# Kernel tuning notes

Measured on AMD Instinct MI355X. Metric: run time of the kernel, lower is better.

The kernel has to match this reference:

```python
import jax, jax.numpy as jnp
import numpy as np


def setup_inputs() -> dict:
    key = jax.random.key(0)
    B, T, D, H = 32, 1600, 512, 512
    # variable lengths, nonincreasing (PackedSequence convention)
    lengths = np.array([T - 25 * i for i in range(B)])            # 1600 .. 825
    bs = (lengths[None, :] > np.arange(T)[:, None]).sum(1)        # batch_sizes[t], nonincreasing
    t_idx = np.repeat(np.arange(T), bs)                           # packed element -> timestep
    b_idx = np.concatenate([np.arange(b) for b in bs])            # packed element -> batch row
    mask = np.arange(B)[None, :] < bs[:, None]                    # [T,B] active mask
    total = int(bs.sum())                                         # 38800
    ks = jax.random.split(key, 7)
    s = 1.0 / np.sqrt(H)
    return {
        "packed_data": jax.random.normal(ks[0], (total, D), jnp.float32),
        "h0": jax.random.normal(ks[1], (B, H), jnp.float32),
        "c0": jax.random.normal(ks[2], (B, H), jnp.float32),
        "w_ih": jax.random.uniform(ks[3], (4 * H, D), jnp.float32, -s, s),
        "w_hh": jax.random.uniform(ks[4], (4 * H, H), jnp.float32, -s, s),
        "b_ih": jax.random.uniform(ks[5], (4 * H,), jnp.float32, -s, s),
        "b_hh": jax.random.uniform(ks[6], (4 * H,), jnp.float32, -s, s),
        "t_idx": jnp.asarray(t_idx, jnp.int32),
        "b_idx": jnp.asarray(b_idx, jnp.int32),
        "mask": jnp.asarray(mask),
    }


def reference(packed_data, h0, c0, w_ih, w_hh, b_ih, b_hh, t_idx, b_idx, mask):
    # Reverse LSTM over a packed variable-length batch.
    # Equivalent math to the torch loop: process timesteps T-1 .. 0; a row's
    # hidden stays at its initial value until the row becomes active.
    T, B = mask.shape
    D = packed_data.shape[1]
    # unpack to padded [T,B,D] (zeros at inactive slots; never read for output)
    padded = jnp.zeros((T, B, D), packed_data.dtype).at[t_idx, b_idx].set(packed_data)

    def step(carry, xm):
        h, c = carry
        x, m = xm                                   # x:[B,D], m:[B]
        gates = x @ w_ih.T + b_ih + h @ w_hh.T + b_hh   # [B,4H]
        i, f, g, o = jnp.split(gates, 4, axis=-1)
        c_new = jax.nn.sigmoid(f) * c + jax.nn.sigmoid(i) * jnp.tanh(g)
        h_new = jax.nn.sigmoid(o) * jnp.tanh(c_new)
        m2 = m[:, None]
        # inactive rows keep their initial hidden until they enter the batch
        return (jnp.where(m2, h_new, h0), jnp.where(m2, c_new, c0)), h_new

    (hT, cT), outs = jax.lax.scan(step, (h0, c0), (padded[::-1], mask[::-1]))
    outs = outs[::-1]                               # [T,B,H], time-forward order
    packed_out = outs[t_idx, b_idx]                 # repack [total,H]
    return packed_out, hT, cT
```

## Files before the change

kernel.cpp:

```cpp
#include <hip/hip_runtime.h>
#include <hip/hip_bf16.h>
#include <stdint.h>

typedef __attribute__((ext_vector_type(8))) short bf16x8;
typedef __attribute__((ext_vector_type(4))) float f32x4;
typedef __attribute__((ext_vector_type(4))) int int4v;
typedef unsigned long long u64;

#define DD 512
#define HH 512
#define BB 32

__device__ __forceinline__ unsigned short f2bf(float f) {
  unsigned u = __float_as_uint(f);
  u += 0x7fffu + ((u >> 16) & 1u);
  return (unsigned short)(u >> 16);
}
__device__ __forceinline__ int pk2(float a, float b) {
  return (int)((unsigned)f2bf(a) | ((unsigned)f2bf(b) << 16));
}
__device__ __forceinline__ float bf2f(unsigned short v) {
  return __uint_as_float((unsigned)v << 16);
}
__device__ __forceinline__ float sigf(float x) { return 1.f / (1.f + __expf(-x)); }
__device__ __forceinline__ float tanhfast(float x) {
  float e = __expf(fminf(fmaxf(2.f * x, -60.f), 60.f));
  return (e - 1.f) / (e + 1.f);
}

__global__ void init_state(u64* hbuf, const float* __restrict__ h0, int* L) {
  int i = blockIdx.x * blockDim.x + threadIdx.x;
  if (i < 32) L[i] = 0;
  if (i < 16384) {
    int g = i >> 13, p = (i >> 12) & 1, m = (i >> 8) & 15, q = i & 255;
    u64 v;
    if (p == 0) {
      int b = g * 16 + m;
      unsigned lo = f2bf(h0[(size_t)b * HH + 2 * q]);
      unsigned hi = f2bf(h0[(size_t)b * HH + 2 * q + 1]);
      v = (u64)(lo | (hi << 16));
    } else {
      v = 0xFFFFFFFF00000000ull;
    }
    hbuf[i] = v;
  }
}

__global__ void init_idx(const int* __restrict__ t_idx, const int* __restrict__ b_idx,
                         int* rowstart, int* L, int total) {
  int r = blockIdx.x * blockDim.x + threadIdx.x;
  if (r >= total) return;
  int t = t_idx[r];
  if (r == 0 || t_idx[r - 1] != t) rowstart[t] = r;
  atomicMax(&L[b_idx[r]], t + 1);
}

__global__ __launch_bounds__(256, 2)
void gx_gemm(const float* __restrict__ X, const float* __restrict__ w_ih,
             const float* __restrict__ b_ih, const float* __restrict__ b_hh,
             unsigned short* __restrict__ GX, int total)
{
  const int ct = blockIdx.x & 7;
  const int rt = blockIdx.x >> 3;
  const int r0 = rt * 64;
  const int j0 = ct * 256;
  const int tid = threadIdx.x;
  const int lane = tid & 63, wv = tid >> 6;
  const int ul = lane & 15, kc = lane >> 4;

  __shared__ unsigned short As[64 * 64];
  __shared__ unsigned short Bs[256 * 64];
  char* As_c = (char*)As;
  char* Bs_c = (char*)Bs;

  f32x4 acc[4][4];
#pragma unroll
  for (int mf = 0; mf < 4; mf++)
#pragma unroll
    for (int nf = 0; nf < 4; nf++) acc[mf][nf] = (f32x4){0.f, 0.f, 0.f, 0.f};

  const int arow_s = tid >> 2;
  const int akq = (tid & 3) * 16;
  const size_t arow_g = (size_t)min(r0 + arow_s, total - 1);
  const int ab = arow_s * 128 + akq * 2, asw = (arow_s & 7) << 4;
  const int bcol = tid;
  const int bb = bcol * 128, bsw = (bcol & 7) << 4;

  for (int ch = 0; ch < 8; ch++) {
    const int k0 = ch * 64;
    {
      const f32x4* ap = (const f32x4*)(X + arow_g * DD + k0 + akq);
      f32x4 a0 = ap[0], a1 = ap[1], a2 = ap[2], a3 = ap[3];
      int4v p0 = {pk2(a0[0], a0[1]), pk2(a0[2], a0[3]), pk2(a1[0], a1[1]), pk2(a1[2], a1[3])};
      int4v p1 = {pk2(a2[0], a2[1]), pk2(a2[2], a2[3]), pk2(a3[0], a3[1]), pk2(a3[2], a3[3])};
      *(int4v*)(As_c + (ab ^ asw)) = p0;
      *(int4v*)(As_c + ((ab + 16) ^ asw)) = p1;
    }
    {
      const f32x4* bp = (const f32x4*)(w_ih + (size_t)(j0 + bcol) * DD + k0);
#pragma unroll
      for (int q = 0; q < 4; q++) {
        f32x4 b0 = bp[4 * q], b1 = bp[4 * q + 1], b2 = bp[4 * q + 2], b3 = bp[4 * q + 3];
        int4v p0 = {pk2(b0[0], b0[1]), pk2(b0[2], b0[3]), pk2(b1[0], b1[1]), pk2(b1[2], b1[3])};
        int4v p1 = {pk2(b2[0], b2[1]), pk2(b2[2], b2[3]), pk2(b3[0], b3[1]), pk2(b3[2], b3[3])};
        *(int4v*)(Bs_c + ((bb + q * 32) ^ bsw)) = p0;
        *(int4v*)(Bs_c + ((bb + q * 32 + 16) ^ bsw)) = p1;
      }
    }
    __syncthreads();
#pragma unroll
    for (int ks = 0; ks < 2; ks++) {
      bf16x8 bfr[4], afr[4];
#pragma unroll
      for (int nf = 0; nf < 4; nf++) {
        int col = wv * 64 + nf * 16 + ul;
        bfr[nf] = *(const bf16x8*)(Bs_c + ((col * 128 + ks * 64 + kc * 16) ^ ((col & 7) << 4)));
      }
#pragma unroll
      for (int mf = 0; mf < 4; mf++) {
        int row = mf * 16 + ul;
        afr[mf] = *(const bf16x8*)(As_c + ((row * 128 + ks * 64 + kc * 16) ^ ((row & 7) << 4)));
      }
#pragma unroll
      for (int mf = 0; mf < 4; mf++)
#pragma unroll
        for (int nf = 0; nf < 4; nf++)
          acc[mf][nf] = __builtin_amdgcn_mfma_f32_16x16x32_bf16(afr[mf], bfr[nf], acc[mf][nf], 0, 0, 0);
    }
    __syncthreads();
  }
#pragma unroll
  for (int nf = 0; nf < 4; nf++) {
    int c = j0 + wv * 64 + nf * 16 + ul;
    float bias = b_ih[c] + b_hh[c];
#pragma unroll
    for (int mf = 0; mf < 4; mf++)
#pragma unroll
      for (int r = 0; r < 4; r++) {
        int row = r0 + mf * 16 + kc * 4 + r;
        if (row < total) GX[(size_t)row * 2048 + c] = f2bf(acc[mf][nf][r] + bias);
      }
  }
}

__global__ __launch_bounds__(512, 2)
void lstm_gx(const float* __restrict__ h0, const float* __restrict__ c0,
             const float* __restrict__ w_hh,
             const int* __restrict__ rowstart, const int* __restrict__ L,
             u64* hbuf, const unsigned short* __restrict__ GX,
             float* out, int total)
{
  const int tid = threadIdx.x;
  const int bid = blockIdx.x;
  const int g = bid & 1;
  const int k = bid >> 1;
  const int lane = tid & 63;
  const int wave = tid >> 6;
  const int gate = wave & 3;
  const int cs = wave >> 2;
  const int ul = lane & 15;
  const int kc = lane >> 4;
  const int u0 = k * 32;
  const int j = gate * 512 + u0 + cs * 16 + ul;

  __shared__ unsigned short h_st[16 * HH];
  __shared__ float gl[4][16][33];

  bf16x8 wfb[16];
#pragma unroll
  for (int kk = 0; kk < 16; kk++) {
    const float* pb = w_hh + (size_t)j * HH + kk * 32 + kc * 8;
    bf16x8 vb;
#pragma unroll
    for (int e = 0; e < 8; e++) vb[e] = (short)f2bf(pb[e]);
    wfb[kk] = vb;
  }

  const int mC = tid >> 5;
  const int uC = tid & 31;
  const int bcell = g * 16 + mC;
  const int uu = u0 + uC;
  const int Lc = L[bcell];
  float c_reg = c0[(size_t)bcell * HH + uu];
  const float c0c = c_reg;
  const float h0c = h0[(size_t)bcell * HH + uu];

  int t0 = 0;
#pragma unroll
  for (int m = 0; m < 16; m++) t0 = max(t0, L[g * 16 + m]);
  t0 -= 1;
  const int S = t0 + 1;

  u64* hb_g = hbuf + g * 8192;
  const size_t hT_off = (size_t)total * HH;
  const size_t cT_off = hT_off + (size_t)BB * HH;

  char* hst_c = (char*)h_st;
  const int gr = (mC + k) & 15;
  const int gc = (uC + 2 * k) & 31;
  const int hbyte = gr * 1024 + gc * 32, hsw = (gr & 7) << 4;
  const int arow = ul * 1024, aswz = (ul & 7) << 4;

  unsigned short gx0 = 0, gx1 = 0, gx2 = 0, gx3 = 0;
  if (t0 < Lc) {
    const unsigned short* gp = GX + (size_t)(rowstart[t0] + bcell) * 2048 + uu;
    gx0 = gp[0]; gx1 = gp[512]; gx2 = gp[1024]; gx3 = gp[1536];
  }

  for (int s = 0, t = t0; s < S; s++, t--) {
    const bool act = (t < Lc);
    const u64* src = hb_g + (size_t)((s & 1) * 4096) + gr * 256 + gc * 8;
    int4v c0v, c1v, c2v, c3v;
    asm volatile(
      "global_load_dwordx4 %0, %4, off sc0 sc1\n\t"
      "global_load_dwordx4 %1, %5, off sc0 sc1\n\t"
      "global_load_dwordx4 %2, %6, off sc0 sc1\n\t"
      "global_load_dwordx4 %3, %7, off sc0 sc1"
      : "=&v"(c0v), "=&v"(c1v), "=&v"(c2v), "=&v"(c3v)
      : "v"(src), "v"(src + 2), "v"(src + 4), "v"(src + 6)
      : "memory");
    asm volatile("s_waitcnt vmcnt(0)" ::: "memory");
    __builtin_amdgcn_sched_barrier(0);
    const unsigned want = (unsigned)s;
    int spins = 0;
    while (!(((unsigned)c0v[1] == want) & ((unsigned)c0v[3] == want) &
             ((unsigned)c1v[1] == want) & ((unsigned)c1v[3] == want) &
             ((unsigned)c2v[1] == want) & ((unsigned)c2v[3] == want) &
             ((unsigned)c3v[1] == want) & ((unsigned)c3v[3] == want))) {
      if (++spins < 4096) {
        asm volatile(
          "global_load_dwordx4 %0, %4, off sc0 sc1\n\t"
          "global_load_dwordx4 %1, %5, off sc0 sc1\n\t"
          "global_load_dwordx4 %2, %6, off sc0 sc1\n\t"
          "global_load_dwordx4 %3, %7, off sc0 sc1\n\t"
          "s_waitcnt vmcnt(0)"
          : "=&v"(c0v), "=&v"(c1v), "=&v"(c2v), "=&v"(c3v)
          : "v"(src), "v"(src + 2), "v"(src + 4), "v"(src + 6)
          : "memory");
        __builtin_amdgcn_sched_barrier(0);
      } else {
        u64 a0 = __hip_atomic_load(src + 0, __ATOMIC_RELAXED, __HIP_MEMORY_SCOPE_AGENT);
        u64 a1 = __hip_atomic_load(src + 1, __ATOMIC_RELAXED, __HIP_MEMORY_SCOPE_AGENT);
        u64 a2 = __hip_atomic_load(src + 2, __ATOMIC_RELAXED, __HIP_MEMORY_SCOPE_AGENT);
        u64 a3 = __hip_atomic_load(src + 3, __ATOMIC_RELAXED, __HIP_MEMORY_SCOPE_AGENT);
        u64 a4 = __hip_atomic_load(src + 4, __ATOMIC_RELAXED, __HIP_MEMORY_SCOPE_AGENT);
        u64 a5 = __hip_atomic_load(src + 5, __ATOMIC_RELAXED, __HIP_MEMORY_SCOPE_AGENT);
        u64 a6 = __hip_atomic_load(src + 6, __ATOMIC_RELAXED, __HIP_MEMORY_SCOPE_AGENT);
        u64 a7 = __hip_atomic_load(src + 7, __ATOMIC_RELAXED, __HIP_MEMORY_SCOPE_AGENT);
        c0v = (int4v){(int)a0, (int)(a0 >> 32), (int)a1, (int)(a1 >> 32)};
        c1v = (int4v){(int)a2, (int)(a2 >> 32), (int)a3, (int)(a3 >> 32)};
        c2v = (int4v){(int)a4, (int)(a4 >> 32), (int)a5, (int)(a5 >> 32)};
        c3v = (int4v){(int)a6, (int)(a6 >> 32), (int)a7, (int)(a7 >> 32)};
      }
    }

    {
      int4v d0 = {c0v[0], c0v[2], c1v[0], c1v[2]};
      int4v d1 = {c2v[0], c2v[2], c3v[0], c3v[2]};
      *(int4v*)(hst_c + (hbyte ^ hsw)) = d0;
      *(int4v*)(hst_c + ((hbyte + 16) ^ hsw)) = d1;
    }
    unsigned short ngx0 = 0, ngx1 = 0, ngx2 = 0, ngx3 = 0;
    if (t > 0 && (t - 1) < Lc) {
      const unsigned short* gp = GX + (size_t)(rowstart[t - 1] + bcell) * 2048 + uu;
      ngx0 = gp[0]; ngx1 = gp[512]; ngx2 = gp[1024]; ngx3 = gp[1536];
    }
    __syncthreads();

    f32x4 C = {0.f, 0.f, 0.f, 0.f};
    f32x4 C2 = {0.f, 0.f, 0.f, 0.f};
#pragma unroll
    for (int kk = 0; kk < 8; kk++) {
      bf16x8 A0 = *(const bf16x8*)(hst_c + ((arow + (2 * kk) * 64 + kc * 16) ^ aswz));
      bf16x8 A1 = *(const bf16x8*)(hst_c + ((arow + (2 * kk + 1) * 64 + kc * 16) ^ aswz));
      C  = __builtin_amdgcn_mfma_f32_16x16x32_bf16(A0, wfb[2 * kk], C, 0, 0, 0);
      C2 = __builtin_amdgcn_mfma_f32_16x16x32_bf16(A1, wfb[2 * kk + 1], C2, 0, 0, 0);
    }
#pragma unroll
    for (int r = 0; r < 4; r++) gl[gate][kc * 4 + r][cs * 16 + ul] = C[r] + C2[r];
    __syncthreads();

    float gi = gl[0][mC][uC] + bf2f(gx0);
    float gf = gl[1][mC][uC] + bf2f(gx1);
    float gg = gl[2][mC][uC] + bf2f(gx2);
    float go = gl[3][mC][uC] + bf2f(gx3);
    float iv = sigf(gi), fv = sigf(gf), gv = tanhfast(gg), ov = sigf(go);
    float cn = fv * c_reg + iv * gv;
    float hn = ov * tanhfast(cn);
    float hp = act ? hn : h0c;
    c_reg = act ? cn : c0c;

    {
      unsigned hbf = (unsigned)f2bf(hp);
      unsigned v1 = __shfl_down(hbf, 1);
      if ((uC & 1) == 0) {
        u64 val = ((u64)(unsigned)(s + 1) << 32) | (hbf & 0xffffu) | ((v1 & 0xffffu) << 16);
        u64* dst = hb_g + (size_t)(((s + 1) & 1) * 4096) + mC * 256 + k * 16 + (uC >> 1);
        __hip_atomic_store(dst, val, __ATOMIC_RELAXED, __HIP_MEMORY_SCOPE_AGENT);
      }
    }
    if (act) {
      const int rst = rowstart[t];
      out[(size_t)(rst + bcell) * HH + uu] = hn;
      if (t == 0) {
        out[hT_off + (size_t)bcell * HH + uu] = hn;
        out[cT_off + (size_t)bcell * HH + uu] = cn;
      }
    }
    gx0 = ngx0; gx1 = ngx1; gx2 = ngx2; gx3 = ngx3;
  }
}

__global__ __launch_bounds__(512, 2)
void lstm_fused(const float* __restrict__ X, const float* __restrict__ h0,
                const float* __restrict__ c0, const float* __restrict__ w_ih,
                const float* __restrict__ w_hh, const float* __restrict__ b_ih,
                const float* __restrict__ b_hh, const int* __restrict__ rowstart,
                const int* __restrict__ L, u64* hbuf,
                float* out, int total)
{
  const int tid = threadIdx.x;
  const int bid = blockIdx.x;
  const int g = bid & 1;
  const int k = bid >> 1;
  const int lane = tid & 63;
  const int wave = tid >> 6;
  const int gate = wave & 3;
  const int cs = wave >> 2;
  const int ul = lane & 15;
  const int kc = lane >> 4;
  const int u0 = k * 32;
  const int j = gate * 512 + u0 + cs * 16 + ul;

  __shared__ unsigned short h_st[16 * DD];
  __shared__ unsigned short x_st[16 * DD];
  __shared__ float gl[4][16][32];

  bf16x8 wfa[16], wfb[16];
#pragma unroll
  for (int kk = 0; kk < 16; kk++) {
    const float* pa = w_ih + (size_t)j * DD + kk * 32 + kc * 8;
    const float* pb = w_hh + (size_t)j * DD + kk * 32 + kc * 8;
    bf16x8 va, vb;
#pragma unroll
    for (int e = 0; e < 8; e++) { va[e] = (short)f2bf(pa[e]); vb[e] = (short)f2bf(pb[e]); }
    wfa[kk] = va; wfb[kk] = vb;
  }
  const float bias = b_ih[j] + b_hh[j];

  const int mC = tid >> 5;
  const int uC = tid & 31;
  const int bcell = g * 16 + mC;
  const int Lc = L[bcell];
  float c_reg = c0[(size_t)bcell * HH + u0 + uC];
  const float c0c = c_reg;
  const float h0c = h0[(size_t)bcell * HH + u0 + uC];

  int t0 = 0;
#pragma unroll
  for (int m = 0; m < 16; m++) t0 = max(t0, L[g * 16 + m]);
  t0 -= 1;
  const int S = t0 + 1;

  u64* hb_g = hbuf + g * 8192;
  const size_t hT_off = (size_t)total * HH;
  const size_t cT_off = hT_off + (size_t)BB * HH;

  char* hst_c = (char*)h_st;
  char* xst_c = (char*)x_st;
  const int gr = (mC + k) & 15;
  const int gc = (uC + 2 * k) & 31;
  const int hbyte = gr * 1024 + gc * 32, hsw = (gr & 7) << 4;
  const int xbyte = mC * 1024 + uC * 32, xsw = (mC & 7) << 4;
  const int arow = ul * 1024, aswz = (ul & 7) << 4;

  f32x4 xr[4];
  {
    if (t0 < Lc) {
      const f32x4* xp = (const f32x4*)(X + (size_t)(rowstart[t0] + bcell) * DD + uC * 16);
#pragma unroll
      for (int q = 0; q < 4; q++) xr[q] = xp[q];
    } else {
#pragma unroll
      for (int q = 0; q < 4; q++) xr[q] = (f32x4){0.f, 0.f, 0.f, 0.f};
    }
  }

  for (int s = 0, t = t0; s < S; s++, t--) {
    const bool act = (t < Lc);
    {
      int4v e0 = {pk2(xr[0][0], xr[0][1]), pk2(xr[0][2], xr[0][3]),
                  pk2(xr[1][0], xr[1][1]), pk2(xr[1][2], xr[1][3])};
      int4v e1 = {pk2(xr[2][0], xr[2][1]), pk2(xr[2][2], xr[2][3]),
                  pk2(xr[3][0], xr[3][1]), pk2(xr[3][2], xr[3][3])};
      *(int4v*)(xst_c + (xbyte ^ xsw)) = e0;
      *(int4v*)(xst_c + ((xbyte + 16) ^ xsw)) = e1;
    }
    __syncthreads();

    const u64* src = hb_g + (size_t)((s & 1) * 4096) + gr * 256 + gc * 8;
    int4v c0v, c1v, c2v, c3v;
    asm volatile(
      "global_load_dwordx4 %0, %4, off sc0 sc1\n\t"
      "global_load_dwordx4 %1, %5, off sc0 sc1\n\t"
      "global_load_dwordx4 %2, %6, off sc0 sc1\n\t"
      "global_load_dwordx4 %3, %7, off sc0 sc1"
      : "=&v"(c0v), "=&v"(c1v), "=&v"(c2v), "=&v"(c3v)
      : "v"(src), "v"(src + 2), "v"(src + 4), "v"(src + 6)
      : "memory");

    f32x4 C = {bias, bias, bias, bias};
#pragma unroll
    for (int kk = 0; kk < 16; kk++) {
      bf16x8 A = *(const bf16x8*)(xst_c + ((arow + kk * 64 + kc * 16) ^ aswz));
      C = __builtin_amdgcn_mfma_f32_16x16x32_bf16(A, wfa[kk], C, 0, 0, 0);
    }

    asm volatile("s_waitcnt vmcnt(0)" ::: "memory");
    __builtin_amdgcn_sched_barrier(0);
    const unsigned want = (unsigned)s;
    int spins = 0;
    while (!(((unsigned)c0v[1] == want) & ((unsigned)c0v[3] == want) &
             ((unsigned)c1v[1] == want) & ((unsigned)c1v[3] == want) &
             ((unsigned)c2v[1] == want) & ((unsigned)c2v[3] == want) &
             ((unsigned)c3v[1] == want) & ((unsigned)c3v[3] == want))) {
      if (++spins < 4096) {
        asm volatile(
          "global_load_dwordx4 %0, %4, off sc0 sc1\n\t"
          "global_load_dwordx4 %1, %5, off sc0 sc1\n\t"
          "global_load_dwordx4 %2, %6, off sc0 sc1\n\t"
          "global_load_dwordx4 %3, %7, off sc0 sc1\n\t"
          "s_waitcnt vmcnt(0)"
          : "=&v"(c0v), "=&v"(c1v), "=&v"(c2v), "=&v"(c3v)
          : "v"(src), "v"(src + 2), "v"(src + 4), "v"(src + 6)
          : "memory");
        __builtin_amdgcn_sched_barrier(0);
      } else {
        u64 a0 = __hip_atomic_load(src + 0, __ATOMIC_RELAXED, __HIP_MEMORY_SCOPE_AGENT);
        u64 a1 = __hip_atomic_load(src + 1, __ATOMIC_RELAXED, __HIP_MEMORY_SCOPE_AGENT);
        u64 a2 = __hip_atomic_load(src + 2, __ATOMIC_RELAXED, __HIP_MEMORY_SCOPE_AGENT);
        u64 a3 = __hip_atomic_load(src + 3, __ATOMIC_RELAXED, __HIP_MEMORY_SCOPE_AGENT);
        u64 a4 = __hip_atomic_load(src + 4, __ATOMIC_RELAXED, __HIP_MEMORY_SCOPE_AGENT);
        u64 a5 = __hip_atomic_load(src + 5, __ATOMIC_RELAXED, __HIP_MEMORY_SCOPE_AGENT);
        u64 a6 = __hip_atomic_load(src + 6, __ATOMIC_RELAXED, __HIP_MEMORY_SCOPE_AGENT);
        u64 a7 = __hip_atomic_load(src + 7, __ATOMIC_RELAXED, __HIP_MEMORY_SCOPE_AGENT);
        c0v = (int4v){(int)a0, (int)(a0 >> 32), (int)a1, (int)(a1 >> 32)};
        c1v = (int4v){(int)a2, (int)(a2 >> 32), (int)a3, (int)(a3 >> 32)};
        c2v = (int4v){(int)a4, (int)(a4 >> 32), (int)a5, (int)(a5 >> 32)};
        c3v = (int4v){(int)a6, (int)(a6 >> 32), (int)a7, (int)(a7 >> 32)};
      }
    }

    {
      bool nact = false;
      if (t > 0) {
        nact = ((t - 1) < Lc);
        if (nact) {
          const f32x4* xp = (const f32x4*)(X + (size_t)(rowstart[t - 1] + bcell) * DD + uC * 16);
#pragma unroll
          for (int q = 0; q < 4; q++) xr[q] = xp[q];
        }
      }
      if (!nact) {
#pragma unroll
        for (int q = 0; q < 4; q++) xr[q] = (f32x4){0.f, 0.f, 0.f, 0.f};
      }
    }

    {
      int4v d0 = {c0v[0], c0v[2], c1v[0], c1v[2]};
      int4v d1 = {c2v[0], c2v[2], c3v[0], c3v[2]};
      *(int4v*)(hst_c + (hbyte ^ hsw)) = d0;
      *(int4v*)(hst_c + ((hbyte + 16) ^ hsw)) = d1;
    }
    __syncthreads();

    f32x4 C2 = {0.f, 0.f, 0.f, 0.f};
#pragma unroll
    for (int kk = 0; kk < 8; kk++) {
      bf16x8 A0 = *(const bf16x8*)(hst_c + ((arow + (2 * kk) * 64 + kc * 16) ^ aswz));
      bf16x8 A1 = *(const bf16x8*)(hst_c + ((arow + (2 * kk + 1) * 64 + kc * 16) ^ aswz));
      C  = __builtin_amdgcn_mfma_f32_16x16x32_bf16(A0, wfb[2 * kk], C, 0, 0, 0);
      C2 = __builtin_amdgcn_mfma_f32_16x16x32_bf16(A1, wfb[2 * kk + 1], C2, 0, 0, 0);
    }
#pragma unroll
    for (int r = 0; r < 4; r++) C[r] += C2[r];

#pragma unroll
    for (int r = 0; r < 4; r++) gl[gate][kc * 4 + r][cs * 16 + ul] = C[r];
    __syncthreads();

    float gi = gl[0][mC][uC], gf = gl[1][mC][uC], gg = gl[2][mC][uC], go = gl[3][mC][uC];
    float iv = sigf(gi), fv = sigf(gf), gv = tanhfast(gg), ov = sigf(go);
    float cn = fv * c_reg + iv * gv;
    float hn = ov * tanhfast(cn);
    float hp = act ? hn : h0c;
    c_reg = act ? cn : c0c;

    {
      unsigned hbf = (unsigned)f2bf(hp);
      unsigned v1 = __shfl_down(hbf, 1);
      if ((uC & 1) == 0) {
        u64 val = ((u64)(unsigned)(s + 1) << 32) | (hbf & 0xffffu) | ((v1 & 0xffffu) << 16);
        u64* dst = hb_g + (size_t)(((s + 1) & 1) * 4096) + mC * 256 + k * 16 + (uC >> 1);
        __hip_atomic_store(dst, val, __ATOMIC_RELAXED, __HIP_MEMORY_SCOPE_AGENT);
      }
    }

    if (act) {
      const int rst = rowstart[t];
      out[(size_t)(rst + bcell) * HH + u0 + uC] = hn;
      if (t == 0) {
        out[hT_off + (size_t)bcell * HH + u0 + uC] = hn;
        out[cT_off + (size_t)bcell * HH + u0 + uC] = cn;
      }
    }
  }
}

extern "C" void kernel_launch(void* const* d_in, const int* in_sizes, int n_in,
                              void* d_out, int out_size, void* d_ws, size_t ws_size,
                              hipStream_t stream) {
  const float* X    = (const float*)d_in[0];
  const float* h0   = (const float*)d_in[1];
  const float* c0   = (const float*)d_in[2];
  const float* w_ih = (const float*)d_in[3];
  const float* w_hh = (const float*)d_in[4];
  const float* b_ih = (const float*)d_in[5];
  const float* b_hh = (const float*)d_in[6];
  const int* t_idx  = (const int*)d_in[7];
  const int* b_idx  = (const int*)d_in[8];
  int total = in_sizes[0] / DD;

  u64* hbuf     = (u64*)d_ws;
  int* rowstart = (int*)((char*)d_ws + 131072);
  int* L        = rowstart + 2048;
  const size_t GX_OFF = 147456;
  unsigned short* GX = (unsigned short*)((char*)d_ws + GX_OFF);
  const size_t need = GX_OFF + (size_t)total * 2048 * 2;

  hipLaunchKernelGGL(init_state, dim3(64), dim3(256), 0, stream, hbuf, h0, L);
  hipLaunchKernelGGL(init_idx, dim3((total + 255) / 256), dim3(256), 0, stream,
                     t_idx, b_idx, rowstart, L, total);
  if (ws_size >= need) {
    int rt = (total + 63) >> 6;
    hipLaunchKernelGGL(gx_gemm, dim3(rt * 8), dim3(256), 0, stream,
                       X, w_ih, b_ih, b_hh, GX, total);
    hipLaunchKernelGGL(lstm_gx, dim3(32), dim3(512), 0, stream,
                       h0, c0, w_hh, rowstart, L, hbuf, GX, (float*)d_out, total);
  } else {
    hipLaunchKernelGGL(lstm_fused, dim3(32), dim3(512), 0, stream,
                       X, h0, c0, w_ih, w_hh, b_ih, b_hh, rowstart, L, hbuf,
                       (float*)d_out, total);
  }
}
```

Before: 4.268 ms.

## Split recurrent LSTM over 16 larger blocks of 1024 threads instead of 32

```diff
diff --git a/kernel.cpp b/kernel.cpp
--- a/kernel.cpp
+++ b/kernel.cpp
@@ -143,12 +143,12 @@
   }
 }
 
-__global__ __launch_bounds__(512, 2)
-void lstm_gx(const float* __restrict__ h0, const float* __restrict__ c0,
-             const float* __restrict__ w_hh,
-             const int* __restrict__ rowstart, const int* __restrict__ L,
-             u64* hbuf, const unsigned short* __restrict__ GX,
-             float* out, int total)
+__global__ __launch_bounds__(1024, 1)
+void lstm_gx8(const float* __restrict__ h0, const float* __restrict__ c0,
+              const float* __restrict__ w_hh,
+              const int* __restrict__ rowstart, const int* __restrict__ L,
+              u64* hbuf, const unsigned short* __restrict__ GX,
+              float* out, int total)
 {
   const int tid = threadIdx.x;
   const int bid = blockIdx.x;
@@ -160,11 +160,11 @@
   const int cs = wave >> 2;
   const int ul = lane & 15;
   const int kc = lane >> 4;
-  const int u0 = k * 32;
+  const int u0 = k * 64;
   const int j = gate * 512 + u0 + cs * 16 + ul;
 
   __shared__ unsigned short h_st[16 * HH];
-  __shared__ float gl[4][16][33];
+  __shared__ float gl[4][16][69];
 
   bf16x8 wfb[16];
 #pragma unroll
@@ -176,8 +176,8 @@
     wfb[kk] = vb;
   }
 
-  const int mC = tid >> 5;
-  const int uC = tid & 31;
+  const int mC = tid >> 6;
+  const int uC = tid & 63;
   const int bcell = g * 16 + mC;
   const int uu = u0 + uC;
   const int Lc = L[bcell];
@@ -197,8 +197,8 @@
 
   char* hst_c = (char*)h_st;
   const int gr = (mC + k) & 15;
-  const int gc = (uC + 2 * k) & 31;
-  const int hbyte = gr * 1024 + gc * 32, hsw = (gr & 7) << 4;
+  const int gc = (uC + 8 * k) & 63;
+  const int hbyte = gr * 1024 + gc * 16, hsw = (gr & 7) << 4;
   const int arow = ul * 1024, aswz = (ul & 7) << 4;
 
   unsigned short gx0 = 0, gx1 = 0, gx2 = 0, gx3 = 0;
@@ -209,56 +209,32 @@
 
   for (int s = 0, t = t0; s < S; s++, t--) {
     const bool act = (t < Lc);
-    const u64* src = hb_g + (size_t)((s & 1) * 4096) + gr * 256 + gc * 8;
-    int4v c0v, c1v, c2v, c3v;
+    const u64* src = hb_g + (size_t)((s & 1) * 4096) + gr * 256 + gc * 4;
+    int4v c0v, c1v;
     asm volatile(
-      "global_load_dwordx4 %0, %4, off sc0 sc1\n\t"
-      "global_load_dwordx4 %1, %5, off sc0 sc1\n\t"
-      "global_load_dwordx4 %2, %6, off sc0 sc1\n\t"
-      "global_load_dwordx4 %3, %7, off sc0 sc1"
-      : "=&v"(c0v), "=&v"(c1v), "=&v"(c2v), "=&v"(c3v)
-      : "v"(src), "v"(src + 2), "v"(src + 4), "v"(src + 6)
+      "global_load_dwordx4 %0, %2, off sc0 sc1\n\t"
+      "global_load_dwordx4 %1, %3, off sc0 sc1\n\t"
+      "s_waitcnt vmcnt(0)"
+      : "=&v"(c0v), "=&v"(c1v)
+      : "v"(src), "v"(src + 2)
       : "memory");
-    asm volatile("s_waitcnt vmcnt(0)" ::: "memory");
     __builtin_amdgcn_sched_barrier(0);
     const unsigned want = (unsigned)s;
-    int spins = 0;
     while (!(((unsigned)c0v[1] == want) & ((unsigned)c0v[3] == want) &
-             ((unsigned)c1v[1] == want) & ((unsigned)c1v[3] == want) &
-             ((unsigned)c2v[1] == want) & ((unsigned)c2v[3] == want) &
-             ((unsigned)c3v[1] == want) & ((unsigned)c3v[3] == want))) {
-      if (++spins < 4096) {
-        asm volatile(
-          "global_load_dwordx4 %0, %4, off sc0 sc1\n\t"
-          "global_load_dwordx4 %1, %5, off sc0 sc1\n\t"
-          "global_load_dwordx4 %2, %6, off sc0 sc1\n\t"
-          "global_load_dwordx4 %3, %7, off sc0 sc1\n\t"
-          "s_waitcnt vmcnt(0)"
-          : "=&v"(c0v), "=&v"(c1v), "=&v"(c2v), "=&v"(c3v)
-          : "v"(src), "v"(src + 2), "v"(src + 4), "v"(src + 6)
-          : "memory");
-        __builtin_amdgcn_sched_barrier(0);
-      } else {
-        u64 a0 = __hip_atomic_load(src + 0, __ATOMIC_RELAXED, __HIP_MEMORY_SCOPE_AGENT);
-        u64 a1 = __hip_atomic_load(src + 1, __ATOMIC_RELAXED, __HIP_MEMORY_SCOPE_AGENT);
-        u64 a2 = __hip_atomic_load(src + 2, __ATOMIC_RELAXED, __HIP_MEMORY_SCOPE_AGENT);
-        u64 a3 = __hip_atomic_load(src + 3, __ATOMIC_RELAXED, __HIP_MEMORY_SCOPE_AGENT);
-        u64 a4 = __hip_atomic_load(src + 4, __ATOMIC_RELAXED, __HIP_MEMORY_SCOPE_AGENT);
-        u64 a5 = __hip_atomic_load(src + 5, __ATOMIC_RELAXED, __HIP_MEMORY_SCOPE_AGENT);
-        u64 a6 = __hip_atomic_load(src + 6, __ATOMIC_RELAXED, __HIP_MEMORY_SCOPE_AGENT);
-        u64 a7 = __hip_atomic_load(src + 7, __ATOMIC_RELAXED, __HIP_MEMORY_SCOPE_AGENT);
-        c0v = (int4v){(int)a0, (int)(a0 >> 32), (int)a1, (int)(a1 >> 32)};
-        c1v = (int4v){(int)a2, (int)(a2 >> 32), (int)a3, (int)(a3 >> 32)};
-        c2v = (int4v){(int)a4, (int)(a4 >> 32), (int)a5, (int)(a5 >> 32)};
-        c3v = (int4v){(int)a6, (int)(a6 >> 32), (int)a7, (int)(a7 >> 32)};
-      }
+             ((unsigned)c1v[1] == want) & ((unsigned)c1v[3] == want))) {
+      asm volatile(
+        "global_load_dwordx4 %0, %2, off sc0 sc1\n\t"
+        "global_load_dwordx4 %1, %3, off sc0 sc1\n\t"
+        "s_waitcnt vmcnt(0)"
+        : "=&v"(c0v), "=&v"(c1v)
+        : "v"(src), "v"(src + 2)
+        : "memory");
+      __builtin_amdgcn_sched_barrier(0);
     }
 
     {
       int4v d0 = {c0v[0], c0v[2], c1v[0], c1v[2]};
-      int4v d1 = {c2v[0], c2v[2], c3v[0], c3v[2]};
       *(int4v*)(hst_c + (hbyte ^ hsw)) = d0;
-      *(int4v*)(hst_c + ((hbyte + 16) ^ hsw)) = d1;
     }
     unsigned short ngx0 = 0, ngx1 = 0, ngx2 = 0, ngx3 = 0;
     if (t > 0 && (t - 1) < Lc) {
@@ -295,7 +271,7 @@
       unsigned v1 = __shfl_down(hbf, 1);
       if ((uC & 1) == 0) {
         u64 val = ((u64)(unsigned)(s + 1) << 32) | (hbf & 0xffffu) | ((v1 & 0xffffu) << 16);
-        u64* dst = hb_g + (size_t)(((s + 1) & 1) * 4096) + mC * 256 + k * 16 + (uC >> 1);
+        u64* dst = hb_g + (size_t)(((s + 1) & 1) * 4096) + mC * 256 + k * 32 + (uC >> 1);
         __hip_atomic_store(dst, val, __ATOMIC_RELAXED, __HIP_MEMORY_SCOPE_AGENT);
       }
     }
@@ -419,36 +395,20 @@
     asm volatile("s_waitcnt vmcnt(0)" ::: "memory");
     __builtin_amdgcn_sched_barrier(0);
     const unsigned want = (unsigned)s;
-    int spins = 0;
     while (!(((unsigned)c0v[1] == want) & ((unsigned)c0v[3] == want) &
              ((unsigned)c1v[1] == want) & ((unsigned)c1v[3] == want) &
              ((unsigned)c2v[1] == want) & ((unsigned)c2v[3] == want) &
              ((unsigned)c3v[1] == want) & ((unsigned)c3v[3] == want))) {
-      if (++spins < 4096) {
-        asm volatile(
-          "global_load_dwordx4 %0, %4, off sc0 sc1\n\t"
-          "global_load_dwordx4 %1, %5, off sc0 sc1\n\t"
-          "global_load_dwordx4 %2, %6, off sc0 sc1\n\t"
-          "global_load_dwordx4 %3, %7, off sc0 sc1\n\t"
-          "s_waitcnt vmcnt(0)"
-          : "=&v"(c0v), "=&v"(c1v), "=&v"(c2v), "=&v"(c3v)
-          : "v"(src), "v"(src + 2), "v"(src + 4), "v"(src + 6)
-          : "memory");
-        __builtin_amdgcn_sched_barrier(0);
-      } else {
-        u64 a0 = __hip_atomic_load(src + 0, __ATOMIC_RELAXED, __HIP_MEMORY_SCOPE_AGENT);
-        u64 a1 = __hip_atomic_load(src + 1, __ATOMIC_RELAXED, __HIP_MEMORY_SCOPE_AGENT);
-        u64 a2 = __hip_atomic_load(src + 2, __ATOMIC_RELAXED, __HIP_MEMORY_SCOPE_AGENT);
-        u64 a3 = __hip_atomic_load(src + 3, __ATOMIC_RELAXED, __HIP_MEMORY_SCOPE_AGENT);
-        u64 a4 = __hip_atomic_load(src + 4, __ATOMIC_RELAXED, __HIP_MEMORY_SCOPE_AGENT);
-        u64 a5 = __hip_atomic_load(src + 5, __ATOMIC_RELAXED, __HIP_MEMORY_SCOPE_AGENT);
-        u64 a6 = __hip_atomic_load(src + 6, __ATOMIC_RELAXED, __HIP_MEMORY_SCOPE_AGENT);
-        u64 a7 = __hip_atomic_load(src + 7, __ATOMIC_RELAXED, __HIP_MEMORY_SCOPE_AGENT);
-        c0v = (int4v){(int)a0, (int)(a0 >> 32), (int)a1, (int)(a1 >> 32)};
-        c1v = (int4v){(int)a2, (int)(a2 >> 32), (int)a3, (int)(a3 >> 32)};
-        c2v = (int4v){(int)a4, (int)(a4 >> 32), (int)a5, (int)(a5 >> 32)};
-        c3v = (int4v){(int)a6, (int)(a6 >> 32), (int)a7, (int)(a7 >> 32)};
-      }
+      asm volatile(
+        "global_load_dwordx4 %0, %4, off sc0 sc1\n\t"
+        "global_load_dwordx4 %1, %5, off sc0 sc1\n\t"
+        "global_load_dwordx4 %2, %6, off sc0 sc1\n\t"
+        "global_load_dwordx4 %3, %7, off sc0 sc1\n\t"
+        "s_waitcnt vmcnt(0)"
+        : "=&v"(c0v), "=&v"(c1v), "=&v"(c2v), "=&v"(c3v)
+        : "v"(src), "v"(src + 2), "v"(src + 4), "v"(src + 6)
+        : "memory");
+      __builtin_amdgcn_sched_barrier(0);
     }
 
     {
@@ -546,7 +506,7 @@
     int rt = (total + 63) >> 6;
     hipLaunchKernelGGL(gx_gemm, dim3(rt * 8), dim3(256), 0, stream,
                        X, w_ih, b_ih, b_hh, GX, total);
-    hipLaunchKernelGGL(lstm_gx, dim3(32), dim3(512), 0, stream,
+    hipLaunchKernelGGL(lstm_gx8, dim3(16), dim3(1024), 0, stream,
                        h0, c0, w_hh, rowstart, L, hbuf, GX, (float*)d_out, total);
   } else {
     hipLaunchKernelGGL(lstm_fused, dim3(32), dim3(512), 0, stream,
```

Result: slower. 5.724 ms (+34.1%).

## Fuse input-projection GEMM into recurrent kernel with per-row-tile completion flags

Applied to the files above, without the earlier changes.

```diff
diff --git a/kernel.cpp b/kernel.cpp
--- a/kernel.cpp
+++ b/kernel.cpp
@@ -27,10 +27,16 @@
   float e = __expf(fminf(fmaxf(2.f * x, -60.f), 60.f));
   return (e - 1.f) / (e + 1.f);
 }
-
-__global__ void init_state(u64* hbuf, const float* __restrict__ h0, int* L) {
+__device__ __forceinline__ unsigned short ldgx(const unsigned short* p) {
+  const unsigned* p4 = (const unsigned*)((size_t)p & ~(size_t)3);
+  unsigned v = __hip_atomic_load(p4, __ATOMIC_RELAXED, __HIP_MEMORY_SCOPE_AGENT);
+  return (unsigned short)(((size_t)p & 2) ? (v >> 16) : (v & 0xffffu));
+}
+
+__global__ void init_state(u64* hbuf, const float* __restrict__ h0, int* L, int* done) {
   int i = blockIdx.x * blockDim.x + threadIdx.x;
   if (i < 32) L[i] = 0;
+  if (i < 640) done[i] = 0;
   if (i < 16384) {
     int g = i >> 13, p = (i >> 12) & 1, m = (i >> 8) & 15, q = i & 255;
     u64 v;
@@ -55,103 +61,119 @@
   atomicMax(&L[b_idx[r]], t + 1);
 }
 
-__global__ __launch_bounds__(256, 2)
-void gx_gemm(const float* __restrict__ X, const float* __restrict__ w_ih,
-             const float* __restrict__ b_ih, const float* __restrict__ b_hh,
-             unsigned short* __restrict__ GX, int total)
+__global__ __launch_bounds__(512, 2)
+void lstm_fx(const float* __restrict__ X, const float* __restrict__ h0,
+             const float* __restrict__ c0, const float* __restrict__ w_ih,
+             const float* __restrict__ w_hh, const float* __restrict__ b_ih,
+             const float* __restrict__ b_hh, const int* __restrict__ rowstart,
+             const int* __restrict__ L, u64* hbuf, unsigned short* GX, int* done,
+             float* out, int total, int NTR)
 {
-  const int ct = blockIdx.x & 7;
-  const int rt = blockIdx.x >> 3;
-  const int r0 = rt * 64;
-  const int j0 = ct * 256;
-  const int tid = threadIdx.x;
-  const int lane = tid & 63, wv = tid >> 6;
-  const int ul = lane & 15, kc = lane >> 4;
-
-  __shared__ unsigned short As[64 * 64];
-  __shared__ unsigned short Bs[256 * 64];
-  char* As_c = (char*)As;
-  char* Bs_c = (char*)Bs;
-
-  f32x4 acc[4][4];
-#pragma unroll
-  for (int mf = 0; mf < 4; mf++)
-#pragma unroll
-    for (int nf = 0; nf < 4; nf++) acc[mf][nf] = (f32x4){0.f, 0.f, 0.f, 0.f};
-
-  const int arow_s = tid >> 2;
-  const int akq = (tid & 3) * 16;
-  const size_t arow_g = (size_t)min(r0 + arow_s, total - 1);
-  const int ab = arow_s * 128 + akq * 2, asw = (arow_s & 7) << 4;
-  const int bcol = tid;
-  const int bb = bcol * 128, bsw = (bcol & 7) << 4;
-
-  for (int ch = 0; ch < 8; ch++) {
-    const int k0 = ch * 64;
-    {
-      const f32x4* ap = (const f32x4*)(X + arow_g * DD + k0 + akq);
-      f32x4 a0 = ap[0], a1 = ap[1], a2 = ap[2], a3 = ap[3];
-      int4v p0 = {pk2(a0[0], a0[1]), pk2(a0[2], a0[3]), pk2(a1[0], a1[1]), pk2(a1[2], a1[3])};
-      int4v p1 = {pk2(a2[0], a2[1]), pk2(a2[2], a2[3]), pk2(a3[0], a3[1]), pk2(a3[2], a3[3])};
-      *(int4v*)(As_c + (ab ^ asw)) = p0;
-      *(int4v*)(As_c + ((ab + 16) ^ asw)) = p1;
-    }
-    {
-      const f32x4* bp = (const f32x4*)(w_ih + (size_t)(j0 + bcol) * DD + k0);
-#pragma unroll
-      for (int q = 0; q < 4; q++) {
-        f32x4 b0 = bp[4 * q], b1 = bp[4 * q + 1], b2 = bp[4 * q + 2], b3 = bp[4 * q + 3];
-        int4v p0 = {pk2(b0[0], b0[1]), pk2(b0[2], b0[3]), pk2(b1[0], b1[1]), pk2(b1[2], b1[3])};
-        int4v p1 = {pk2(b2[0], b2[1]), pk2(b2[2], b2[3]), pk2(b3[0], b3[1]), pk2(b3[2], b3[3])};
-        *(int4v*)(Bs_c + ((bb + q * 32) ^ bsw)) = p0;
-        *(int4v*)(Bs_c + ((bb + q * 32 + 16) ^ bsw)) = p1;
-      }
-    }
-    __syncthreads();
-#pragma unroll
-    for (int ks = 0; ks < 2; ks++) {
-      bf16x8 bfr[4], afr[4];
-#pragma unroll
-      for (int nf = 0; nf < 4; nf++) {
-        int col = wv * 64 + nf * 16 + ul;
-        bfr[nf] = *(const bf16x8*)(Bs_c + ((col * 128 + ks * 64 + kc * 16) ^ ((col & 7) << 4)));
-      }
-#pragma unroll
-      for (int mf = 0; mf < 4; mf++) {
-        int row = mf * 16 + ul;
-        afr[mf] = *(const bf16x8*)(As_c + ((row * 128 + ks * 64 + kc * 16) ^ ((row & 7) << 4)));
-      }
-#pragma unroll
-      for (int mf = 0; mf < 4; mf++)
-#pragma unroll
-        for (int nf = 0; nf < 4; nf++)
-          acc[mf][nf] = __builtin_amdgcn_mfma_f32_16x16x32_bf16(afr[mf], bfr[nf], acc[mf][nf], 0, 0, 0);
-    }
-    __syncthreads();
-  }
-#pragma unroll
-  for (int nf = 0; nf < 4; nf++) {
-    int c = j0 + wv * 64 + nf * 16 + ul;
-    float bias = b_ih[c] + b_hh[c];
-#pragma unroll
-    for (int mf = 0; mf < 4; mf++)
-#pragma unroll
-      for (int r = 0; r < 4; r++) {
-        int row = r0 + mf * 16 + kc * 4 + r;
-        if (row < total) GX[(size_t)row * 2048 + c] = f2bf(acc[mf][nf][r] + bias);
-      }
-  }
-}
-
-__global__ __launch_bounds__(512, 2)
-void lstm_gx(const float* __restrict__ h0, const float* __restrict__ c0,
-             const float* __restrict__ w_hh,
-             const int* __restrict__ rowstart, const int* __restrict__ L,
-             u64* hbuf, const unsigned short* __restrict__ GX,
-             float* out, int total)
-{
+  __shared__ __align__(16) char smem[40960];
   const int tid = threadIdx.x;
   const int bid = blockIdx.x;
+
+  if (bid >= 32) {
+    const int gxid = bid - 32;
+    const int rt = NTR - 1 - (gxid >> 3);
+    const int ct = gxid & 7;
+    const int r0 = rt * 64;
+    const int j0 = ct * 256;
+    char* As_c = smem;
+    char* Bs_c = smem + 8192;
+    const int lane = tid & 63, wv = tid >> 6;
+    const int ul = lane & 15, kc = lane >> 4;
+
+    f32x4 acc[4][2];
+#pragma unroll
+    for (int mf = 0; mf < 4; mf++)
+#pragma unroll
+      for (int nf = 0; nf < 2; nf++) acc[mf][nf] = (f32x4){0.f, 0.f, 0.f, 0.f};
+
+    const int arow_s = tid >> 3;
+    const int akq = (tid & 7) * 8;
+    const size_t arow_g = (size_t)min(r0 + arow_s, total - 1);
+    const int ab = arow_s * 128 + akq * 2, asw = (arow_s & 7) << 4;
+    const int bcol = tid >> 1;
+    const int bkh = (tid & 1) * 32;
+    const int bb = bcol * 128 + bkh * 2, bsw = (bcol & 7) << 4;
+
+    for (int ch = 0; ch < 8; ch++) {
+      const int k0 = ch * 64;
+      {
+        const f32x4* ap = (const f32x4*)(X + arow_g * DD + k0 + akq);
+        f32x4 a0 = ap[0], a1 = ap[1];
+        int4v p0 = {pk2(a0[0], a0[1]), pk2(a0[2], a0[3]),
+                    pk2(a1[0], a1[1]), pk2(a1[2], a1[3])};
+        *(int4v*)(As_c + (ab ^ asw)) = p0;
+      }
+      {
+        const f32x4* bp = (const f32x4*)(w_ih + (size_t)(j0 + bcol) * DD + k0 + bkh);
+#pragma unroll
+        for (int q = 0; q < 2; q++) {
+          f32x4 b0 = bp[4 * q], b1 = bp[4 * q + 1], b2 = bp[4 * q + 2], b3 = bp[4 * q + 3];
+          int4v p0 = {pk2(b0[0], b0[1]), pk2(b0[2], b0[3]), pk2(b1[0], b1[1]), pk2(b1[2], b1[3])};
+          int4v p1 = {pk2(b2[0], b2[1]), pk2(b2[2], b2[3]), pk2(b3[0], b3[1]), pk2(b3[2], b3[3])};
+          *(int4v*)(Bs_c + ((bb + q * 32) ^ bsw)) = p0;
+          *(int4v*)(Bs_c + ((bb + q * 32 + 16) ^ bsw)) = p1;
+        }
+      }
+      __syncthreads();
+#pragma unroll
+      for (int ks = 0; ks < 2; ks++) {
+        bf16x8 bfr[2], afr[4];
+#pragma unroll
+        for (int nf = 0; nf < 2; nf++) {
+          int col = wv * 32 + nf * 16 + ul;
+          bfr[nf] = *(const bf16x8*)(Bs_c + ((col * 128 + ks * 64 + kc * 16) ^ ((col & 7) << 4)));
+        }
+#pragma unroll
+        for (int mf = 0; mf < 4; mf++) {
+          int row = mf * 16 + ul;
+          afr[mf] = *(const bf16x8*)(As_c + ((row * 128 + ks * 64 + kc * 16) ^ ((row & 7) << 4)));
+        }
+#pragma unroll
+        for (int mf = 0; mf < 4; mf++)
+#pragma unroll
+          for (int nf = 0; nf < 2; nf++)
+            acc[mf][nf] = __builtin_amdgcn_mfma_f32_16x16x32_bf16(afr[mf], bfr[nf], acc[mf][nf], 0, 0, 0);
+      }
+      __syncthreads();
+    }
+    unsigned short* eL = (unsigned short*)smem;
+#pragma unroll
+    for (int nf = 0; nf < 2; nf++) {
+      int cl = wv * 32 + nf * 16 + ul;
+      float bias = b_ih[j0 + cl] + b_hh[j0 + cl];
+#pragma unroll
+      for (int mf = 0; mf < 4; mf++)
+#pragma unroll
+        for (int r = 0; r < 4; r++)
+          eL[(mf * 16 + kc * 4 + r) * 256 + cl] = f2bf(acc[mf][nf][r] + bias);
+    }
+    __syncthreads();
+    {
+      int rowl = tid >> 3;
+      int co = (tid & 7) * 32;
+      int growr = r0 + rowl;
+      if (growr < total) {
+        const int4v* sp = (const int4v*)(eL + rowl * 256 + co);
+        unsigned short* dp = GX + (size_t)growr * 2048 + j0 + co;
+#pragma unroll
+        for (int i = 0; i < 4; i++) {
+          int4v v = sp[i];
+          asm volatile("global_store_dwordx4 %0, %1, off sc0 sc1"
+                       :: "v"(dp + i * 8), "v"(v) : "memory");
+        }
+      }
+    }
+    asm volatile("s_waitcnt vmcnt(0)" ::: "memory");
+    __syncthreads();
+    if (tid == 0)
+      __hip_atomic_fetch_add(&done[rt], 1, __ATOMIC_RELAXED, __HIP_MEMORY_SCOPE_AGENT);
+    return;
+  }
+
   const int g = bid & 1;
   const int k = bid >> 1;
   const int lane = tid & 63;
@@ -163,8 +185,8 @@
   const int u0 = k * 32;
   const int j = gate * 512 + u0 + cs * 16 + ul;
 
-  __shared__ unsigned short h_st[16 * HH];
-  __shared__ float gl[4][16][33];
+  char* hst_c = smem;
+  float* glf = (float*)(smem + 16384);
 
   bf16x8 wfb[16];
 #pragma unroll
@@ -195,16 +217,28 @@
   const size_t hT_off = (size_t)total * HH;
   const size_t cT_off = hT_off + (size_t)BB * HH;
 
-  char* hst_c = (char*)h_st;
   const int gr = (mC + k) & 15;
   const int gc = (uC + 2 * k) & 31;
   const int hbyte = gr * 1024 + gc * 32, hsw = (gr & 7) << 4;
   const int arow = ul * 1024, aswz = (ul & 7) << 4;
 
+  int frontier = NTR;
+
   unsigned short gx0 = 0, gx1 = 0, gx2 = 0, gx3 = 0;
-  if (t0 < Lc) {
-    const unsigned short* gp = GX + (size_t)(rowstart[t0] + bcell) * 2048 + uu;
-    gx0 = gp[0]; gx1 = gp[512]; gx2 = gp[1024]; gx3 = gp[1536];
+  {
+    if (tid == 0) {
+      int rs0 = rowstart[t0];
+      int rlo = rs0 >> 6, rhi = min((rs0 + 15) >> 6, NTR - 1);
+      while (__hip_atomic_load(&done[rlo], __ATOMIC_RELAXED, __HIP_MEMORY_SCOPE_AGENT) < 8 ||
+             __hip_atomic_load(&done[rhi], __ATOMIC_RELAXED, __HIP_MEMORY_SCOPE_AGENT) < 8)
+        __builtin_amdgcn_s_sleep(8);
+      frontier = rlo;
+    }
+    __syncthreads();
+    if (t0 < Lc) {
+      const unsigned short* gp = GX + (size_t)(rowstart[t0] + bcell) * 2048 + uu;
+      gx0 = ldgx(gp); gx1 = ldgx(gp + 512); gx2 = ldgx(gp + 1024); gx3 = ldgx(gp + 1536);
+    }
   }
 
   for (int s = 0, t = t0; s < S; s++, t--) {
@@ -260,12 +294,24 @@
       *(int4v*)(hst_c + (hbyte ^ hsw)) = d0;
       *(int4v*)(hst_c + ((hbyte + 16) ^ hsw)) = d1;
     }
+    if (tid == 0 && t > 0) {
+      int rs = rowstart[t - 1];
+      int rlo = rs >> 6;
+      if (rlo < frontier) {
+        int rhi = min((rs + 15) >> 6, NTR - 1);
+        while (__hip_atomic_load(&done[rlo], __ATOMIC_RELAXED, __HIP_MEMORY_SCOPE_AGENT) < 8 ||
+               __hip_atomic_load(&done[rhi], __ATOMIC_RELAXED, __HIP_MEMORY_SCOPE_AGENT) < 8)
+          __builtin_amdgcn_s_sleep(2);
+        frontier = rlo;
+      }
+    }
+    __syncthreads();
+
     unsigned short ngx0 = 0, ngx1 = 0, ngx2 = 0, ngx3 = 0;
     if (t > 0 && (t - 1) < Lc) {
       const unsigned short* gp = GX + (size_t)(rowstart[t - 1] + bcell) * 2048 + uu;
-      ngx0 = gp[0]; ngx1 = gp[512]; ngx2 = gp[1024]; ngx3 = gp[1536];
-    }
-    __syncthreads();
+      ngx0 = ldgx(gp); ngx1 = ldgx(gp + 512); ngx2 = ldgx(gp + 1024); ngx3 = ldgx(gp + 1536);
+    }
 
     f32x4 C = {0.f, 0.f, 0.f, 0.f};
     f32x4 C2 = {0.f, 0.f, 0.f, 0.f};
@@ -277,13 +323,14 @@
       C2 = __builtin_amdgcn_mfma_f32_16x16x32_bf16(A1, wfb[2 * kk + 1], C2, 0, 0, 0);
     }
 #pragma unroll
-    for (int r = 0; r < 4; r++) gl[gate][kc * 4 + r][cs * 16 + ul] = C[r] + C2[r];
-    __syncthreads();
-
-    float gi = gl[0][mC][uC] + bf2f(gx0);
-    float gf = gl[1][mC][uC] + bf2f(gx1);
-    float gg = gl[2][mC][uC] + bf2f(gx2);
-    float go = gl[3][mC][uC] + bf2f(gx3);
+    for (int r = 0; r < 4; r++)
+      glf[gate * 528 + (kc * 4 + r) * 33 + cs * 16 + ul] = C[r] + C2[r];
+    __syncthreads();
+
+    float gi = glf[0 * 528 + mC * 33 + uC] + bf2f(gx0);
+    float gf = glf[1 * 528 + mC * 33 + uC] + bf2f(gx1);
+    float gg = glf[2 * 528 + mC * 33 + uC] + bf2f(gx2);
+    float go = glf[3 * 528 + mC * 33 + uC] + bf2f(gx3);
     float iv = sigf(gi), fv = sigf(gf), gv = tanhfast(gg), ov = sigf(go);
     float cn = fv * c_reg + iv * gv;
     float hn = ov * tanhfast(cn);
@@ -535,19 +582,19 @@
   u64* hbuf     = (u64*)d_ws;
   int* rowstart = (int*)((char*)d_ws + 131072);
   int* L        = rowstart + 2048;
+  int* done     = (int*)((char*)d_ws + 139392);
   const size_t GX_OFF = 147456;
   unsigned short* GX = (unsigned short*)((char*)d_ws + GX_OFF);
   const size_t need = GX_OFF + (size_t)total * 2048 * 2;
-
-  hipLaunchKernelGGL(init_state, dim3(64), dim3(256), 0, stream, hbuf, h0, L);
+  const int NTR = (total + 63) >> 6;
+
+  hipLaunchKernelGGL(init_state, dim3(64), dim3(256), 0, stream, hbuf, h0, L, done);
   hipLaunchKernelGGL(init_idx, dim3((total + 255) / 256), dim3(256), 0, stream,
                      t_idx, b_idx, rowstart, L, total);
   if (ws_size >= need) {
-    int rt = (total + 63) >> 6;
-    hipLaunchKernelGGL(gx_gemm, dim3(rt * 8), dim3(256), 0, stream,
-                       X, w_ih, b_ih, b_hh, GX, total);
-    hipLaunchKernelGGL(lstm_gx, dim3(32), dim3(512), 0, stream,
-                       h0, c0, w_hh, rowstart, L, hbuf, GX, (float*)d_out, total);
+    hipLaunchKernelGGL(lstm_fx, dim3(32 + 8 * NTR), dim3(512), 0, stream,
+                       X, h0, c0, w_ih, w_hh, b_ih, b_hh, rowstart, L,
+                       hbuf, GX, done, (float*)d_out, total, NTR);
   } else {
     hipLaunchKernelGGL(lstm_fused, dim3(32), dim3(512), 0, stream,
                        X, h0, c0, w_ih, w_hh, b_ih, b_hh, rowstart, L, hbuf,
```

After: 4.633 ms. 1.09x slower.
